# Kernel tuning notes

Hardware: AMD Instinct MI355X
Metric: run time of the kernel (lower is better)

The kernel has to match this reference:

```python
import jax, jax.numpy as jnp
import numpy as np

B, S, H, NH = 2, 2048, 1024, 16
HD = H // NH  # head_dim = 64


def setup_inputs() -> dict:
    key = jax.random.key(0)
    k1, k2, k3 = jax.random.split(key, 3)
    x = jax.random.normal(k1, (B, S, H), dtype=jnp.float32)
    # additive causal mask: 0 on/below diagonal, -1e9 above
    causal = jnp.tril(jnp.ones((S, S), dtype=bool))
    mask = jnp.where(causal, 0.0, -1e9).astype(jnp.float32)[None, None, :, :]
    # fan-in scaled init like flax Dense default (lecun_normal)
    W_qkv = jax.random.normal(k2, (H, 3 * H), dtype=jnp.float32) / np.sqrt(H)
    W_out = jax.random.normal(k3, (H, H), dtype=jnp.float32) / np.sqrt(H)
    return {"x": x, "mask": mask, "W_qkv": W_qkv, "W_out": W_out}


def reference(x, mask, W_qkv, W_out):
    b, s, _ = x.shape
    qkv = jnp.einsum('bsh,hf->bsf', x, W_qkv)  # [B,S,3H]
    q, k, v = jnp.split(qkv, 3, axis=-1)
    q = q.reshape(b, s, NH, HD)
    k = k.reshape(b, s, NH, HD)
    v = v.reshape(b, s, NH, HD)
    scores = jnp.einsum('bqhd,bkhd->bhqk', q, k) / jnp.sqrt(jnp.float32(HD))
    scores = scores + mask
    attn = jax.nn.softmax(scores, axis=-1)
    y = jnp.einsum('bhqk,bkhd->bqhd', attn, v).reshape(b, s, H)
    return jnp.einsum('bsh,ho->bso', y, W_out)
```

## Files before the change

kernel.cpp:

```cpp
#include <hip/hip_runtime.h>

#define B_ 2
#define S_ 2048
#define H_ 1024
#define NH_ 16
#define HD_ 64

typedef short s16x8 __attribute__((ext_vector_type(8)));
typedef float f32x4 __attribute__((ext_vector_type(4)));

__device__ __forceinline__ ushort f2bf(float f) {
  union { float f; unsigned u; } v;
  v.f = f;
  unsigned r = (v.u + 0x7fffu + ((v.u >> 16) & 1u)) >> 16;
  return (ushort)r;
}

__device__ __forceinline__ void gload16(const void* g, void* l) {
  typedef const __attribute__((address_space(1))) unsigned int* gp_t;
  typedef __attribute__((address_space(3))) unsigned int* lp_t;
  __builtin_amdgcn_global_load_lds((gp_t)g, (lp_t)l, 16, 0, 0);
}

__global__ __launch_bounds__(256) void k_prep(const float* __restrict__ x,
                                              ushort* __restrict__ xb,
                                              const float* __restrict__ Wqkv,
                                              ushort* __restrict__ wqkvT,
                                              const float* __restrict__ Wout,
                                              ushort* __restrict__ woutT) {
  __shared__ ushort tile[32][33];
  const int bid = blockIdx.x;
  if (bid < 4096) {
    int i = bid * 256 + threadIdx.x;
    float4 v = ((const float4*)x)[i];
    ushort4 o;
    o.x = f2bf(v.x); o.y = f2bf(v.y); o.z = f2bf(v.z); o.w = f2bf(v.w);
    ((ushort4*)xb)[i] = o;
    return;
  }
  const float* in;
  ushort* out;
  int R = 1024, C, t;
  if (bid < 7168) { in = Wqkv; out = wqkvT; C = 3072; t = bid - 4096; }
  else            { in = Wout; out = woutT; C = 1024; t = bid - 7168; }
  int nbx = C >> 5;
  int c0 = (t % nbx) * 32, r0 = (t / nbx) * 32;
  int tr = threadIdx.x >> 5, tc = threadIdx.x & 31;
#pragma unroll
  for (int i = 0; i < 4; ++i)
    tile[tr + 8 * i][tc] = f2bf(in[(size_t)(r0 + tr + 8 * i) * C + c0 + tc]);
  __syncthreads();
#pragma unroll
  for (int i = 0; i < 4; ++i)
    out[(size_t)(c0 + tr + 8 * i) * R + r0 + tc] = tile[tc][tr + 8 * i];
}

template <int MODE>
__global__ __launch_bounds__(512, 2) void k_gemm(const ushort* __restrict__ A,
                                                 const ushort* __restrict__ Bt,
                                                 void* __restrict__ out0,
                                                 ushort* __restrict__ outK,
                                                 ushort* __restrict__ outV,
                                                 int Kdim, int Ndim) {
  __shared__ __align__(16) ushort As[2][256 * 64];
  __shared__ __align__(16) ushort Bs[2][256 * 64];
  const int nwg = gridDim.x * gridDim.y;
  const int id = blockIdx.y * gridDim.x + blockIdx.x;
  const int sid = (id & 7) * (nwg >> 3) + (id >> 3);
  const int m0 = (sid / gridDim.x) * 256, n0 = (sid % gridDim.x) * 256;
  const int tid = threadIdx.x, lane = tid & 63, w = tid >> 6;
  const int g = lane >> 4, c = lane & 15;
  const int wm = w >> 2, wn = w & 3;
  f32x4 acc[8][4] = {};

  const int srow = tid >> 3;
  const int csrc = (tid & 7) ^ (srow & 7);
  const ushort* ag = A + (size_t)(m0 + srow) * Kdim + csrc * 8;
  const ushort* bg = Bt + (size_t)(n0 + srow) * Kdim + csrc * 8;
  const int nT = Kdim >> 6;

#define STRIPE(gp, ro, T_, dst) \
  gload16((gp) + (size_t)(ro) * Kdim + (T_) * 64, (dst) + tid * 8)

  STRIPE(ag, 0, 0, As[0]); STRIPE(ag, 64, 0, As[0] + 4096);
  STRIPE(bg, 0, 0, Bs[0]); STRIPE(bg, 64, 0, Bs[0] + 4096);
  STRIPE(bg, 128, 0, Bs[0] + 8192); STRIPE(bg, 192, 0, Bs[0] + 12288);
  STRIPE(ag, 128, 0, As[0] + 8192); STRIPE(ag, 192, 0, As[0] + 12288);
  asm volatile("s_waitcnt vmcnt(4)" ::: "memory");
  __builtin_amdgcn_s_barrier();
  __builtin_amdgcn_sched_barrier(0);

#pragma unroll 1
  for (int t = 0; t < nT; ++t) {
    const char* Ab = (const char*)As[t & 1];
    const char* Bb = (const char*)Bs[t & 1];
    const bool stg = (t + 1 < nT);
    const int T2 = t + 1, bf2 = T2 & 1;
#pragma unroll
    for (int q = 0; q < 4; ++q) {
      const int ih = q >> 1, jh = q & 1;
      s16x8 af[4][2], bfr[2][2];
#pragma unroll
      for (int i2 = 0; i2 < 4; ++i2) {
        int row = ih * 128 + wm * 64 + i2 * 16 + c;
#pragma unroll
        for (int kk = 0; kk < 2; ++kk) {
          int ch = g + kk * 4;
          af[i2][kk] = *(const s16x8*)(Ab + row * 128 + ((ch ^ (row & 7)) << 4));
        }
      }
#pragma unroll
      for (int j2 = 0; j2 < 2; ++j2) {
        int row = jh * 128 + wn * 32 + j2 * 16 + c;
#pragma unroll
        for (int kk = 0; kk < 2; ++kk) {
          int ch = g + kk * 4;
          bfr[j2][kk] = *(const s16x8*)(Bb + row * 128 + ((ch ^ (row & 7)) << 4));
        }
      }
      if (stg) {
        if (q == 0) { STRIPE(ag, 0, T2, As[bf2]);          STRIPE(ag, 64, T2, As[bf2] + 4096); }
        if (q == 1) { STRIPE(bg, 0, T2, Bs[bf2]);          STRIPE(bg, 64, T2, Bs[bf2] + 4096); }
        if (q == 2) { STRIPE(bg, 128, T2, Bs[bf2] + 8192); STRIPE(bg, 192, T2, Bs[bf2] + 12288); }
        if (q == 3) { STRIPE(ag, 128, T2, As[bf2] + 8192); STRIPE(ag, 192, T2, As[bf2] + 12288); }
      }
      __builtin_amdgcn_s_barrier();
      asm volatile("s_waitcnt lgkmcnt(0)" ::: "memory");
      __builtin_amdgcn_sched_barrier(0);
      __builtin_amdgcn_s_setprio(1);
#pragma unroll
      for (int i2 = 0; i2 < 4; ++i2)
#pragma unroll
        for (int j2 = 0; j2 < 2; ++j2)
#pragma unroll
          for (int kk = 0; kk < 2; ++kk)
            acc[ih * 4 + i2][jh * 2 + j2] = __builtin_amdgcn_mfma_f32_16x16x32_bf16(
                af[i2][kk], bfr[j2][kk], acc[ih * 4 + i2][jh * 2 + j2], 0, 0, 0);
      __builtin_amdgcn_s_setprio(0);
      if (stg) {
        if (q != 2) asm volatile("s_waitcnt vmcnt(4)" ::: "memory");
      } else {
        if (q == 0) asm volatile("s_waitcnt vmcnt(2)" ::: "memory");
        else if (q == 1) asm volatile("s_waitcnt vmcnt(0)" ::: "memory");
      }
      __builtin_amdgcn_s_barrier();
      __builtin_amdgcn_sched_barrier(0);
    }
  }
#undef STRIPE

  {
    if (n0 < 1024) {
      const float ALPHA = 0.18033688f;
      ushort* outQ = (ushort*)out0;
#pragma unroll
      for (int i = 0; i < 8; ++i) {
        int mb = m0 + (i >> 2) * 128 + wm * 64 + (i & 3) * 16 + g * 4;
#pragma unroll
        for (int j = 0; j < 4; ++j) {
          int n = n0 + (j >> 1) * 128 + wn * 32 + (j & 1) * 16 + c;
#pragma unroll
          for (int r = 0; r < 4; ++r)
            outQ[(size_t)(mb + r) * 1024 + n] = f2bf(acc[i][j][r] * ALPHA);
        }
      }
    } else if (n0 < 2048) {
#pragma unroll
      for (int i = 0; i < 8; ++i) {
        int mb = m0 + (i >> 2) * 128 + wm * 64 + (i & 3) * 16 + g * 4;
#pragma unroll
        for (int j = 0; j < 4; ++j) {
          int n = n0 - 1024 + (j >> 1) * 128 + wn * 32 + (j & 1) * 16 + c;
#pragma unroll
          for (int r = 0; r < 4; ++r)
            outK[(size_t)(mb + r) * 1024 + n] = f2bf(acc[i][j][r]);
        }
      }
    } else {
#pragma unroll
      for (int i = 0; i < 8; ++i) {
        int mb = m0 + (i >> 2) * 128 + wm * 64 + (i & 3) * 16 + g * 4;
        int bidx = mb >> 11;
        int s = mb & 2047;
#pragma unroll
        for (int j = 0; j < 4; ++j) {
          int nv = n0 - 2048 + (j >> 1) * 128 + wn * 32 + (j & 1) * 16 + c;
          int h = nv >> 6, d = nv & 63;
          ushort4 pk;
          pk.x = f2bf(acc[i][j][0]);
          pk.y = f2bf(acc[i][j][1]);
          pk.z = f2bf(acc[i][j][2]);
          pk.w = f2bf(acc[i][j][3]);
          *(ushort4*)(outV + ((size_t)((bidx * 16 + h) * 64 + d)) * 2048 + s) = pk;
        }
      }
    }
  }
}

__global__ __launch_bounds__(256) void k_gemm_o(const ushort* __restrict__ A,
                                                const ushort* __restrict__ Bt,
                                                float* __restrict__ out,
                                                int Kdim, int Ndim) {
  __shared__ __align__(16) ushort As[2][128 * 64];
  __shared__ __align__(16) ushort Bs[2][128 * 64];
  const int nwg = gridDim.x * gridDim.y;
  const int id = blockIdx.y * gridDim.x + blockIdx.x;
  const int sid = (id & 7) * (nwg >> 3) + (id >> 3);
  const int m0 = (sid / gridDim.x) * 128, n0 = (sid % gridDim.x) * 128;
  const int tid = threadIdx.x, lane = tid & 63, w = tid >> 6;
  const int g = lane >> 4, c = lane & 15;
  const int wr = w >> 1, wc = w & 1;
  f32x4 acc[4][4] = {};
  const int trow = tid >> 3, tcol = tid & 7;
  const ushort* ag = A + (size_t)(m0 + trow) * Kdim + tcol * 8;
  const ushort* bg = Bt + (size_t)(n0 + trow) * Kdim + tcol * 8;

#define STG_O(bf, k0)                                        \
  do {                                                       \
    _Pragma("unroll") for (int i_ = 0; i_ < 4; ++i_) {       \
      gload16(ag + (k0) + i_ * 32 * Kdim, As[bf] + tid * 8 + i_ * 2048); \
      gload16(bg + (k0) + i_ * 32 * Kdim, Bs[bf] + tid * 8 + i_ * 2048); \
    }                                                        \
  } while (0)

  const int nk = Kdim >> 6;
  STG_O(0, 0);
  asm volatile("s_waitcnt vmcnt(0)" ::: "memory");
  __builtin_amdgcn_s_barrier();
  __builtin_amdgcn_sched_barrier(0);

  int buf = 0;
#pragma unroll 1
  for (int t = 0; t < nk; ++t) {
    if (t + 1 < nk) STG_O(buf ^ 1, (t + 1) * 64);
#pragma unroll
    for (int kk = 0; kk < 64; kk += 32) {
      s16x8 af[4], bfr[4];
#pragma unroll
      for (int i = 0; i < 4; ++i)
        af[i] = *(const s16x8*)(As[buf] + (wr * 64 + i * 16 + c) * 64 + kk + g * 8);
#pragma unroll
      for (int i = 0; i < 4; ++i)
        bfr[i] = *(const s16x8*)(Bs[buf] + (wc * 64 + i * 16 + c) * 64 + kk + g * 8);
      __builtin_amdgcn_s_setprio(1);
#pragma unroll
      for (int i = 0; i < 4; ++i)
#pragma unroll
        for (int j = 0; j < 4; ++j)
          acc[i][j] = __builtin_amdgcn_mfma_f32_16x16x32_bf16(af[i], bfr[j], acc[i][j], 0, 0, 0);
      __builtin_amdgcn_s_setprio(0);
    }
    asm volatile("s_waitcnt vmcnt(0)" ::: "memory");
    __builtin_amdgcn_s_barrier();
    __builtin_amdgcn_sched_barrier(0);
    buf ^= 1;
  }
#undef STG_O

#pragma unroll
  for (int i = 0; i < 4; ++i) {
    int mb = m0 + wr * 64 + i * 16 + g * 4;
#pragma unroll
    for (int j = 0; j < 4; ++j) {
      int n = n0 + wc * 64 + j * 16 + c;
#pragma unroll
      for (int r = 0; r < 4; ++r)
        out[(size_t)(mb + r) * Ndim + n] = acc[i][j][r];
    }
  }
}

__global__ __launch_bounds__(128) void k_attn(const ushort* __restrict__ Qb,
                                              const ushort* __restrict__ Kb,
                                              const ushort* __restrict__ Vt,
                                              ushort* __restrict__ Yb) {
  __shared__ __align__(16) ushort Ks[2][64 * 64];
  __shared__ __align__(16) ushort Vs[2][64 * 64];
  __shared__ __align__(16) unsigned int Pp[2][16 * 32];
  const int fid = blockIdx.x;
  const int wid = (fid & 7) * 128 + (fid >> 3);
  const int bh = wid >> 5;
  const int j = wid & 31;
  const int b = bh >> 4, h = bh & 15;
  const int tid = threadIdx.x, w = tid >> 6, lane = tid & 63;
  const int g = lane >> 4, c = lane & 15;
  char* pb = (char*)(&Pp[w][0]);

  const int trow = tid >> 3, tcol = tid & 7;
  const int csrc = tcol ^ (trow & 7);
  const ushort* kgb = Kb + (size_t)(b * S_ + trow) * H_ + h * HD_ + csrc * 8;
  const ushort* vgb = Vt + (size_t)(bh * HD_ + trow) * S_ + csrc * 8;

#define STAGE(bf, tile)                                              \
  do {                                                               \
    int ks_ = (tile) * 64;                                           \
    gload16(kgb + (size_t)(ks_ +  0) * H_, Ks[bf] +    0 + tid * 8); \
    gload16(kgb + (size_t)(ks_ + 16) * H_, Ks[bf] + 1024 + tid * 8); \
    gload16(kgb + (size_t)(ks_ + 32) * H_, Ks[bf] + 2048 + tid * 8); \
    gload16(kgb + (size_t)(ks_ + 48) * H_, Ks[bf] + 3072 + tid * 8); \
    gload16(vgb + ks_ +  0 * S_, Vs[bf] +    0 + tid * 8);           \
    gload16(vgb + ks_ + 16 * S_, Vs[bf] + 1024 + tid * 8);           \
    gload16(vgb + ks_ + 32 * S_, Vs[bf] + 2048 + tid * 8);           \
    gload16(vgb + ks_ + 48 * S_, Vs[bf] + 3072 + tid * 8);           \
  } while (0)

#pragma unroll 1
  for (int half = 0; half < 2; ++half) {
    const int qc = half ? (63 - j) : j;
    const int q0 = qc * 32;
    const int nt = (qc >> 1) + 1;
    const int qw = q0 + w * 16;

    s16x8 qf[2];
#pragma unroll
    for (int dc = 0; dc < 2; ++dc)
      qf[dc] = *(const s16x8*)(Qb + (size_t)(b * S_ + qw + c) * H_ +
                               h * HD_ + dc * 32 + g * 8);

    f32x4 oacc[4] = {};
    float m = -1e30f, lp = 0.f;

    STAGE(0, 0);
    asm volatile("s_waitcnt vmcnt(0)" ::: "memory");
    __builtin_amdgcn_s_barrier();
    __builtin_amdgcn_sched_barrier(0);

    int buf = 0;
#pragma unroll 1
    for (int it = 0; it < nt; ++it) {
      const int ks = it * 64;
      if (it + 1 < nt) STAGE(buf ^ 1, it + 1);

      f32x4 sacc[4] = {};
      __builtin_amdgcn_s_setprio(1);
#pragma unroll
      for (int dc = 0; dc < 2; ++dc) {
#pragma unroll
        for (int kt = 0; kt < 4; ++kt) {
          int R = kt * 16 + c;
          int cc = dc * 4 + g;
          s16x8 kf = *(const s16x8*)((const char*)Ks[buf] + R * 128 + ((cc ^ (R & 7)) << 4));
          sacc[kt] = __builtin_amdgcn_mfma_f32_16x16x32_bf16(kf, qf[dc], sacc[kt], 0, 0, 0);
        }
      }
      __builtin_amdgcn_s_setprio(0);

      if (it == nt - 1) {
        int q = qw + c;
#pragma unroll
        for (int kt = 0; kt < 4; ++kt)
#pragma unroll
          for (int r = 0; r < 4; ++r)
            if (ks + kt * 16 + g * 4 + r > q) sacc[kt][r] = -1e30f;
      }

      float t0 = fmaxf(fmaxf(sacc[0][0], sacc[0][1]), fmaxf(sacc[0][2], sacc[0][3]));
      float t1 = fmaxf(fmaxf(sacc[1][0], sacc[1][1]), fmaxf(sacc[1][2], sacc[1][3]));
      float t2 = fmaxf(fmaxf(sacc[2][0], sacc[2][1]), fmaxf(sacc[2][2], sacc[2][3]));
      float t3 = fmaxf(fmaxf(sacc[3][0], sacc[3][1]), fmaxf(sacc[3][2], sacc[3][3]));
      float t = fmaxf(fmaxf(t0, t1), fmaxf(t2, t3));
      t = fmaxf(t, __shfl_xor(t, 16));
      t = fmaxf(t, __shfl_xor(t, 32));

      if (__any(t > m + 8.0f)) {
        float mnew = fmaxf(m, t);
        float sc = __builtin_amdgcn_exp2f(m - mnew);
        m = mnew;
        lp *= sc;
        float scq[4];
#pragma unroll
        for (int r = 0; r < 4; ++r) scq[r] = __shfl(sc, g * 4 + r);
#pragma unroll
        for (int dt = 0; dt < 4; ++dt)
#pragma unroll
          for (int r = 0; r < 4; ++r) oacc[dt][r] *= scq[r];
      }

      float p[4][4];
      float rs = 0.f;
#pragma unroll
      for (int kt = 0; kt < 4; ++kt)
#pragma unroll
        for (int r = 0; r < 4; ++r) {
          p[kt][r] = __builtin_amdgcn_exp2f(sacc[kt][r] - m);
          rs += p[kt][r];
        }
      lp += rs;
      unsigned int pw[8];
#pragma unroll
      for (int kt = 0; kt < 4; ++kt) {
        asm("v_cvt_pk_bf16_f32 %0, %1, %2" : "=v"(pw[kt * 2 + 0]) : "v"(p[kt][0]), "v"(p[kt][1]));
        asm("v_cvt_pk_bf16_f32 %0, %1, %2" : "=v"(pw[kt * 2 + 1]) : "v"(p[kt][2]), "v"(p[kt][3]));
      }
#pragma unroll
      for (int kt = 0; kt < 4; ++kt) {
        int qd = kt * 2 + (g >> 1);
        *(uint2*)(pb + c * 128 + ((qd ^ (c & 7)) << 4) + ((g & 1) << 3)) =
            make_uint2(pw[kt * 2], pw[kt * 2 + 1]);
      }
      asm volatile("s_waitcnt lgkmcnt(0)" ::: "memory");
      __builtin_amdgcn_sched_barrier(0);

      __builtin_amdgcn_s_setprio(1);
#pragma unroll
      for (int kc = 0; kc < 2; ++kc) {
        int qd = kc * 4 + g;
        s16x8 pf = *(const s16x8*)(pb + c * 128 + ((qd ^ (c & 7)) << 4));
        int cc = kc * 4 + g;
#pragma unroll
        for (int dt = 0; dt < 4; ++dt) {
          int R = dt * 16 + c;
          s16x8 vf = *(const s16x8*)((const char*)Vs[buf] + R * 128 + ((cc ^ (R & 7)) << 4));
          oacc[dt] = __builtin_amdgcn_mfma_f32_16x16x32_bf16(pf, vf, oacc[dt], 0, 0, 0);
        }
      }
      __builtin_amdgcn_s_setprio(0);

      asm volatile("s_waitcnt vmcnt(0)" ::: "memory");
      __builtin_amdgcn_s_barrier();
      __builtin_amdgcn_sched_barrier(0);
      buf ^= 1;
    }

    float lt = lp;
    lt += __shfl_xor(lt, 16);
    lt += __shfl_xor(lt, 32);
    float rq[4];
#pragma unroll
    for (int r = 0; r < 4; ++r) rq[r] = 1.0f / __shfl(lt, g * 4 + r);
#pragma unroll
    for (int dt = 0; dt < 4; ++dt)
#pragma unroll
      for (int r = 0; r < 4; ++r) {
        int s = qw + g * 4 + r;
        Yb[(size_t)(b * S_ + s) * H_ + h * HD_ + dt * 16 + c] = f2bf(oacc[dt][r] * rq[r]);
      }
  }
#undef STAGE
}

extern "C" void kernel_launch(void* const* d_in, const int* in_sizes, int n_in,
                              void* d_out, int out_size, void* d_ws, size_t ws_size,
                              hipStream_t stream) {
  (void)in_sizes; (void)n_in; (void)out_size; (void)ws_size;
  const float* x = (const float*)d_in[0];
  const float* Wqkv = (const float*)d_in[2];
  const float* Wout = (const float*)d_in[3];
  float* out = (float*)d_out;

  char* ws = (char*)d_ws;
  ushort* xb    = (ushort*)(ws + 0);
  ushort* wqkvT = (ushort*)(ws + 8388608);
  ushort* woutT = (ushort*)(ws + 14680064);
  ushort* Qb    = (ushort*)(ws + 16777216);
  ushort* Kb    = (ushort*)(ws + 25165824);
  ushort* Vtb   = (ushort*)(ws + 33554432);
  ushort* Yb    = (ushort*)(ws + 41943040);

  k_prep<<<dim3(8192), dim3(256), 0, stream>>>(x, xb, Wqkv, wqkvT, Wout, woutT);
  k_gemm<0><<<dim3(12, 16), dim3(512), 0, stream>>>(xb, wqkvT, (void*)Qb, Kb, Vtb, 1024, 3072);
  k_attn<<<dim3(1024), dim3(128), 0, stream>>>(Qb, Kb, Vtb, Yb);
  k_gemm_o<<<dim3(8, 32), dim3(256), 0, stream>>>(Yb, woutT, out, 1024, 1024);
}
```

Before: 204.9 us.

## Process two 16-row query tiles per wave in attention to reuse K/V tiles

Each wave now handles 32 query rows (two 16-row MFMA tiles) instead of 16, so each workgroup covers 64 queries and the grid shrinks from 1024 to 512 blocks. Every K and V fragment read from LDS feeds two MFMAs, and each staged 64-key tile is shared by twice as many queries, which cuts global and LDS traffic per unit of work. The cost is roughly double the accumulator registers per wave, which may lower occupancy, and fewer blocks, which reduces parallelism and coarsens causal load balancing.

After: 222.7 us. +8.7%, slower.

```diff
diff --git a/kernel.cpp b/kernel.cpp
--- a/kernel.cpp
+++ b/kernel.cpp
@@ -277,11 +277,11 @@
                                               ushort* __restrict__ Yb) {
   __shared__ __align__(16) ushort Ks[2][64 * 64];
   __shared__ __align__(16) ushort Vs[2][64 * 64];
-  __shared__ __align__(16) unsigned int Pp[2][16 * 32];
+  __shared__ __align__(16) unsigned int Pp[2][32 * 32];
   const int fid = blockIdx.x;
-  const int wid = (fid & 7) * 128 + (fid >> 3);
-  const int bh = wid >> 5;
-  const int j = wid & 31;
+  const int wid = (fid & 7) * 64 + (fid >> 3);
+  const int bh = wid >> 4;
+  const int j = wid & 15;
   const int b = bh >> 4, h = bh & 15;
   const int tid = threadIdx.x, w = tid >> 6, lane = tid & 63;
   const int g = lane >> 4, c = lane & 15;
@@ -307,19 +307,21 @@
 
 #pragma unroll 1
   for (int half = 0; half < 2; ++half) {
-    const int qc = half ? (63 - j) : j;
-    const int q0 = qc * 32;
-    const int nt = (qc >> 1) + 1;
-    const int qw = q0 + w * 16;
-
-    s16x8 qf[2];
-#pragma unroll
-    for (int dc = 0; dc < 2; ++dc)
-      qf[dc] = *(const s16x8*)(Qb + (size_t)(b * S_ + qw + c) * H_ +
-                               h * HD_ + dc * 32 + g * 8);
-
-    f32x4 oacc[4] = {};
-    float m = -1e30f, lp = 0.f;
+    const int qc = half ? (31 - j) : j;
+    const int q0 = qc * 64;
+    const int nt = qc + 1;
+    const int qw = q0 + w * 32;
+
+    s16x8 qf[2][2];
+#pragma unroll
+    for (int qt = 0; qt < 2; ++qt)
+#pragma unroll
+      for (int dc = 0; dc < 2; ++dc)
+        qf[qt][dc] = *(const s16x8*)(Qb + (size_t)(b * S_ + qw + qt * 16 + c) * H_ +
+                                     h * HD_ + dc * 32 + g * 8);
+
+    f32x4 oacc[2][4] = {};
+    float m[2] = {-1e30f, -1e30f}, lp[2] = {0.f, 0.f};
 
     STAGE(0, 0);
     asm volatile("s_waitcnt vmcnt(0)" ::: "memory");
@@ -332,7 +334,7 @@
       const int ks = it * 64;
       if (it + 1 < nt) STAGE(buf ^ 1, it + 1);
 
-      f32x4 sacc[4] = {};
+      f32x4 sacc[2][4] = {};
       __builtin_amdgcn_s_setprio(1);
 #pragma unroll
       for (int dc = 0; dc < 2; ++dc) {
@@ -341,63 +343,69 @@
           int R = kt * 16 + c;
           int cc = dc * 4 + g;
           s16x8 kf = *(const s16x8*)((const char*)Ks[buf] + R * 128 + ((cc ^ (R & 7)) << 4));
-          sacc[kt] = __builtin_amdgcn_mfma_f32_16x16x32_bf16(kf, qf[dc], sacc[kt], 0, 0, 0);
+#pragma unroll
+          for (int qt = 0; qt < 2; ++qt)
+            sacc[qt][kt] = __builtin_amdgcn_mfma_f32_16x16x32_bf16(kf, qf[qt][dc], sacc[qt][kt], 0, 0, 0);
         }
       }
       __builtin_amdgcn_s_setprio(0);
 
       if (it == nt - 1) {
-        int q = qw + c;
-#pragma unroll
-        for (int kt = 0; kt < 4; ++kt)
-#pragma unroll
-          for (int r = 0; r < 4; ++r)
-            if (ks + kt * 16 + g * 4 + r > q) sacc[kt][r] = -1e30f;
-      }
-
-      float t0 = fmaxf(fmaxf(sacc[0][0], sacc[0][1]), fmaxf(sacc[0][2], sacc[0][3]));
-      float t1 = fmaxf(fmaxf(sacc[1][0], sacc[1][1]), fmaxf(sacc[1][2], sacc[1][3]));
-      float t2 = fmaxf(fmaxf(sacc[2][0], sacc[2][1]), fmaxf(sacc[2][2], sacc[2][3]));
-      float t3 = fmaxf(fmaxf(sacc[3][0], sacc[3][1]), fmaxf(sacc[3][2], sacc[3][3]));
-      float t = fmaxf(fmaxf(t0, t1), fmaxf(t2, t3));
-      t = fmaxf(t, __shfl_xor(t, 16));
-      t = fmaxf(t, __shfl_xor(t, 32));
-
-      if (__any(t > m + 8.0f)) {
-        float mnew = fmaxf(m, t);
-        float sc = __builtin_amdgcn_exp2f(m - mnew);
-        m = mnew;
-        lp *= sc;
-        float scq[4];
-#pragma unroll
-        for (int r = 0; r < 4; ++r) scq[r] = __shfl(sc, g * 4 + r);
-#pragma unroll
-        for (int dt = 0; dt < 4; ++dt)
-#pragma unroll
-          for (int r = 0; r < 4; ++r) oacc[dt][r] *= scq[r];
-      }
-
-      float p[4][4];
-      float rs = 0.f;
-#pragma unroll
-      for (int kt = 0; kt < 4; ++kt)
-#pragma unroll
-        for (int r = 0; r < 4; ++r) {
-          p[kt][r] = __builtin_amdgcn_exp2f(sacc[kt][r] - m);
-          rs += p[kt][r];
-        }
-      lp += rs;
-      unsigned int pw[8];
-#pragma unroll
-      for (int kt = 0; kt < 4; ++kt) {
-        asm("v_cvt_pk_bf16_f32 %0, %1, %2" : "=v"(pw[kt * 2 + 0]) : "v"(p[kt][0]), "v"(p[kt][1]));
-        asm("v_cvt_pk_bf16_f32 %0, %1, %2" : "=v"(pw[kt * 2 + 1]) : "v"(p[kt][2]), "v"(p[kt][3]));
-      }
-#pragma unroll
-      for (int kt = 0; kt < 4; ++kt) {
-        int qd = kt * 2 + (g >> 1);
-        *(uint2*)(pb + c * 128 + ((qd ^ (c & 7)) << 4) + ((g & 1) << 3)) =
-            make_uint2(pw[kt * 2], pw[kt * 2 + 1]);
+#pragma unroll
+        for (int qt = 0; qt < 2; ++qt) {
+          int q = qw + qt * 16 + c;
+#pragma unroll
+          for (int kt = 0; kt < 4; ++kt)
+#pragma unroll
+            for (int r = 0; r < 4; ++r)
+              if (ks + kt * 16 + g * 4 + r > q) sacc[qt][kt][r] = -1e30f;
+        }
+      }
+
+#pragma unroll
+      for (int qt = 0; qt < 2; ++qt) {
+        float t0 = fmaxf(fmaxf(sacc[qt][0][0], sacc[qt][0][1]), fmaxf(sacc[qt][0][2], sacc[qt][0][3]));
+        float t1 = fmaxf(fmaxf(sacc[qt][1][0], sacc[qt][1][1]), fmaxf(sacc[qt][1][2], sacc[qt][1][3]));
+        float t2 = fmaxf(fmaxf(sacc[qt][2][0], sacc[qt][2][1]), fmaxf(sacc[qt][2][2], sacc[qt][2][3]));
+        float t3 = fmaxf(fmaxf(sacc[qt][3][0], sacc[qt][3][1]), fmaxf(sacc[qt][3][2], sacc[qt][3][3]));
+        float t = fmaxf(fmaxf(t0, t1), fmaxf(t2, t3));
+        t = fmaxf(t, __shfl_xor(t, 16));
+        t = fmaxf(t, __shfl_xor(t, 32));
+
+        if (__any(t > m[qt] + 8.0f)) {
+          float mnew = fmaxf(m[qt], t);
+          float sc = __builtin_amdgcn_exp2f(m[qt] - mnew);
+          m[qt] = mnew;
+          lp[qt] *= sc;
+          float scq[4];
+#pragma unroll
+          for (int r = 0; r < 4; ++r) scq[r] = __shfl(sc, g * 4 + r);
+#pragma unroll
+          for (int dt = 0; dt < 4; ++dt)
+#pragma unroll
+            for (int r = 0; r < 4; ++r) oacc[qt][dt][r] *= scq[r];
+        }
+
+        float rs = 0.f;
+        unsigned int pw[8];
+#pragma unroll
+        for (int kt = 0; kt < 4; ++kt) {
+          float p0 = __builtin_amdgcn_exp2f(sacc[qt][kt][0] - m[qt]);
+          float p1 = __builtin_amdgcn_exp2f(sacc[qt][kt][1] - m[qt]);
+          float p2 = __builtin_amdgcn_exp2f(sacc[qt][kt][2] - m[qt]);
+          float p3 = __builtin_amdgcn_exp2f(sacc[qt][kt][3] - m[qt]);
+          rs += (p0 + p1) + (p2 + p3);
+          asm("v_cvt_pk_bf16_f32 %0, %1, %2" : "=v"(pw[kt * 2 + 0]) : "v"(p0), "v"(p1));
+          asm("v_cvt_pk_bf16_f32 %0, %1, %2" : "=v"(pw[kt * 2 + 1]) : "v"(p2), "v"(p3));
+        }
+        lp[qt] += rs;
+        int prow = qt * 16 + c;
+#pragma unroll
+        for (int kt = 0; kt < 4; ++kt) {
+          int qd = kt * 2 + (g >> 1);
+          *(uint2*)(pb + prow * 128 + ((qd ^ (prow & 7)) << 4) + ((g & 1) << 3)) =
+              make_uint2(pw[kt * 2], pw[kt * 2 + 1]);
+        }
       }
       asm volatile("s_waitcnt lgkmcnt(0)" ::: "memory");
       __builtin_amdgcn_sched_barrier(0);
@@ -405,14 +413,21 @@
       __builtin_amdgcn_s_setprio(1);
 #pragma unroll
       for (int kc = 0; kc < 2; ++kc) {
-        int qd = kc * 4 + g;
-        s16x8 pf = *(const s16x8*)(pb + c * 128 + ((qd ^ (c & 7)) << 4));
+        s16x8 pf[2];
+#pragma unroll
+        for (int qt = 0; qt < 2; ++qt) {
+          int prow = qt * 16 + c;
+          int qd = kc * 4 + g;
+          pf[qt] = *(const s16x8*)(pb + prow * 128 + ((qd ^ (prow & 7)) << 4));
+        }
         int cc = kc * 4 + g;
 #pragma unroll
         for (int dt = 0; dt < 4; ++dt) {
           int R = dt * 16 + c;
           s16x8 vf = *(const s16x8*)((const char*)Vs[buf] + R * 128 + ((cc ^ (R & 7)) << 4));
-          oacc[dt] = __builtin_amdgcn_mfma_f32_16x16x32_bf16(pf, vf, oacc[dt], 0, 0, 0);
+#pragma unroll
+          for (int qt = 0; qt < 2; ++qt)
+            oacc[qt][dt] = __builtin_amdgcn_mfma_f32_16x16x32_bf16(pf[qt], vf, oacc[qt][dt], 0, 0, 0);
         }
       }
       __builtin_amdgcn_s_setprio(0);
@@ -423,19 +438,22 @@
       buf ^= 1;
     }
 
-    float lt = lp;
-    lt += __shfl_xor(lt, 16);
-    lt += __shfl_xor(lt, 32);
-    float rq[4];
-#pragma unroll
-    for (int r = 0; r < 4; ++r) rq[r] = 1.0f / __shfl(lt, g * 4 + r);
-#pragma unroll
-    for (int dt = 0; dt < 4; ++dt)
-#pragma unroll
-      for (int r = 0; r < 4; ++r) {
-        int s = qw + g * 4 + r;
-        Yb[(size_t)(b * S_ + s) * H_ + h * HD_ + dt * 16 + c] = f2bf(oacc[dt][r] * rq[r]);
-      }
+#pragma unroll
+    for (int qt = 0; qt < 2; ++qt) {
+      float lt = lp[qt];
+      lt += __shfl_xor(lt, 16);
+      lt += __shfl_xor(lt, 32);
+      float rq[4];
+#pragma unroll
+      for (int r = 0; r < 4; ++r) rq[r] = 1.0f / __shfl(lt, g * 4 + r);
+#pragma unroll
+      for (int dt = 0; dt < 4; ++dt)
+#pragma unroll
+        for (int r = 0; r < 4; ++r) {
+          int s = qw + qt * 16 + g * 4 + r;
+          Yb[(size_t)(b * S_ + s) * H_ + h * HD_ + dt * 16 + c] = f2bf(oacc[qt][dt][r] * rq[r]);
+        }
+    }
   }
 #undef STAGE
 }
@@ -460,6 +478,6 @@
 
   k_prep<<<dim3(8192), dim3(256), 0, stream>>>(x, xb, Wqkv, wqkvT, Wout, woutT);
   k_gemm<0><<<dim3(12, 16), dim3(512), 0, stream>>>(xb, wqkvT, (void*)Qb, Kb, Vtb, 1024, 3072);
-  k_attn<<<dim3(1024), dim3(128), 0, stream>>>(Qb, Kb, Vtb, Yb);
+  k_attn<<<dim3(512), dim3(128), 0, stream>>>(Qb, Kb, Vtb, Yb);
   k_gemm_o<<<dim3(8, 32), dim3(256), 0, stream>>>(Yb, woutT, out, 1024, 1024);
 }
```
